# Optimization experiments

Hardware: AMD Instinct MI355X
Metric: run time of the kernel (lower is better)

Reference implementation:

```python
import jax, jax.numpy as jnp
import numpy as np

DIM = 1024
HEADS = 16
HEAD_DIM = DIM // HEADS
SCALE = HEAD_DIM ** -0.5
EPS = 1e-5


def layernorm(x, g, b):
    mu = jnp.mean(x, axis=-1, keepdims=True)
    var = jnp.mean((x - mu) ** 2, axis=-1, keepdims=True)
    return (x - mu) * jax.lax.rsqrt(var + EPS) * g + b


def setup_inputs() -> dict:
    key = jax.random.key(0)
    ks = jax.random.split(key, 12)
    B, N = 2, 2048
    s = DIM ** -0.5
    return {
        "q": jax.random.normal(ks[0], (B, N, DIM), jnp.float32),
        "k": jax.random.normal(ks[1], (B, N, DIM), jnp.float32),
        "v": jax.random.normal(ks[2], (B, N, DIM), jnp.float32),
        "gq": jnp.ones((DIM,), jnp.float32), "bq_ln": jnp.zeros((DIM,), jnp.float32),
        "gk": jnp.ones((DIM,), jnp.float32), "bk_ln": jnp.zeros((DIM,), jnp.float32),
        "gv": jnp.ones((DIM,), jnp.float32), "bv_ln": jnp.zeros((DIM,), jnp.float32),
        "Wq": jax.random.normal(ks[3], (DIM, DIM), jnp.float32) * s,
        "bq": jnp.zeros((DIM,), jnp.float32),
        "Wk": jax.random.normal(ks[4], (DIM, DIM), jnp.float32) * s,
        "bk": jnp.zeros((DIM,), jnp.float32),
        "Wv": jax.random.normal(ks[5], (DIM, DIM), jnp.float32) * s,
        "bv": jnp.zeros((DIM,), jnp.float32),
        "Wp": jax.random.normal(ks[6], (DIM, DIM), jnp.float32) * s,
        "bp": jnp.zeros((DIM,), jnp.float32),
    }


def reference(q, k, v, gq, bq_ln, gk, bk_ln, gv, bv_ln, Wq, bq, Wk, bk, Wv, bv, Wp, bp):
    B, Nq, C = q.shape
    Nk, Nv = k.shape[1], v.shape[1]
    qn = layernorm(q, gq, bq_ln)
    kn = layernorm(k, gk, bk_ln)
    vn = layernorm(v, gv, bv_ln)
    # project and split heads -> [B, H, N, hd]
    qh = (qn @ Wq + bq).reshape(B, Nq, HEADS, HEAD_DIM).transpose(0, 2, 1, 3)
    kh = (kn @ Wk + bk).reshape(B, Nk, HEADS, HEAD_DIM).transpose(0, 2, 1, 3)
    vh = (vn @ Wv + bv).reshape(B, Nv, HEADS, HEAD_DIM).transpose(0, 2, 1, 3)
    attn = jnp.einsum("bhqd,bhkd->bhqk", qh, kh) * SCALE
    attn = jax.nn.softmax(attn, axis=-1)
    out = jnp.einsum("bhqk,bhkd->bhqd", attn, vh)
    out = out.transpose(0, 2, 1, 3).reshape(B, Nq, C)
    out = out @ Wp + bp
    return (out, kh, vh)
```

## Files before the change

kernel.cpp:

```cpp
#include <hip/hip_runtime.h>
#include <cstdint>

#define DIMC 1024
#define NSEQ 2048
#define BATCH 2
#define HEADS 16
#define HD 64
#define MROWS (BATCH * NSEQ)

typedef unsigned short u16;
typedef unsigned int u32;
typedef __attribute__((ext_vector_type(8))) short bf16x8;
typedef __attribute__((ext_vector_type(4))) float f32x4;

#if __has_builtin(__builtin_amdgcn_exp2f)
#define EXP2(x) __builtin_amdgcn_exp2f(x)
#else
#define EXP2(x) exp2f(x)
#endif

__device__ __forceinline__ u16 f2bf(float f) {
  union { float f; u32 u; } v; v.f = f;
  u32 u = v.u;
  return (u16)((u + 0x7fffu + ((u >> 16) & 1u)) >> 16);
}
__device__ __forceinline__ u32 pack_rne(float a, float b) {
  return (u32)f2bf(a) | ((u32)f2bf(b) << 16);
}
__device__ __forceinline__ u32 pack_trunc(float a, float b) {
  union { float f; u32 u; } x, y; x.f = a; y.f = b;
  return (x.u >> 16) | (y.u & 0xffff0000u);
}
__device__ __forceinline__ void gload_lds16(const void* g, void* l) {
  __builtin_amdgcn_global_load_lds((const __attribute__((address_space(1))) void*)g,
                                   (__attribute__((address_space(3))) void*)l, 16, 0, 0);
}

__global__ __launch_bounds__(256)
void prep(const float* __restrict__ q, const float* __restrict__ k,
          const float* __restrict__ v,
          const float* __restrict__ gq, const float* __restrict__ bq,
          const float* __restrict__ gk, const float* __restrict__ bk,
          const float* __restrict__ gv, const float* __restrict__ bv,
          const float* __restrict__ w0, const float* __restrict__ w1,
          const float* __restrict__ w2, const float* __restrict__ w3,
          u16* __restrict__ xn, u16* __restrict__ wtout) {
  __shared__ float rs[4], rs2[4];
  __shared__ float tile[32][33];
  int tid = threadIdx.x;
  if (blockIdx.x < 3 * MROWS) {
    int rowid = blockIdx.x;
    int tensor = rowid >> 12;
    int r = rowid & 4095;
    const float *src, *g, *b;
    if (tensor == 0)      { src = q; g = gq; b = bq; }
    else if (tensor == 1) { src = k; g = gk; b = bk; }
    else                  { src = v; g = gv; b = bv; }
    src += (size_t)r * DIMC;
    u16* dst = xn + (size_t)tensor * MROWS * DIMC + (size_t)r * DIMC;
    float4 x = ((const float4*)src)[tid];
    float s  = x.x + x.y + x.z + x.w;
    float s2 = x.x*x.x + x.y*x.y + x.z*x.z + x.w*x.w;
    #pragma unroll
    for (int m = 1; m < 64; m <<= 1) { s += __shfl_xor(s, m); s2 += __shfl_xor(s2, m); }
    int wave = tid >> 6, lane = tid & 63;
    if (lane == 0) { rs[wave] = s; rs2[wave] = s2; }
    __syncthreads();
    s  = rs[0] + rs[1] + rs[2] + rs[3];
    s2 = rs2[0] + rs2[1] + rs2[2] + rs2[3];
    float mu  = s * (1.0f / DIMC);
    float var = s2 * (1.0f / DIMC) - mu * mu;
    float inv = rsqrtf(var + 1e-5f);
    float4 gg = ((const float4*)g)[tid];
    float4 bb = ((const float4*)b)[tid];
    uint2 o;
    o.x = pack_rne((x.x - mu) * inv * gg.x + bb.x, (x.y - mu) * inv * gg.y + bb.y);
    o.y = pack_rne((x.z - mu) * inv * gg.z + bb.z, (x.w - mu) * inv * gg.w + bb.w);
    ((uint2*)dst)[tid] = o;
  } else {
    int blk = blockIdx.x - 3 * MROWS;
    int widx = blk >> 10, t = blk & 1023;
    int ti = t >> 5, tj = t & 31;
    const float* W = (widx == 0) ? w0 : (widx == 1) ? w1 : (widx == 2) ? w2 : w3;
    u16* O = wtout + (size_t)widx * DIMC * DIMC;
    int tx = tid & 31, ty = tid >> 5;
    #pragma unroll
    for (int rr = 0; rr < 32; rr += 8)
      tile[ty + rr][tx] = W[(size_t)(ti * 32 + ty + rr) * DIMC + tj * 32 + tx];
    __syncthreads();
    #pragma unroll
    for (int rr = 0; rr < 32; rr += 8)
      O[(size_t)(tj * 32 + ty + rr) * DIMC + ti * 32 + tx] = f2bf(tile[tx][ty + rr]);
  }
}

__global__ __launch_bounds__(256)
void qkv_gemm(const u16* __restrict__ xn, const u16* __restrict__ wt,
              const float* __restrict__ bq, const float* __restrict__ bk,
              const float* __restrict__ bv,
              float* __restrict__ out, u16* __restrict__ qh,
              u16* __restrict__ khb, u16* __restrict__ vtb) {
  __shared__ u16 smem[128 * 136];
  u16* As = smem;
  u16* Bs = smem + 4096;
  u16* Ls = smem;
  const int z = blockIdx.z;
  const u16* A  = xn + (size_t)z * MROWS * DIMC;
  const u16* Bt = wt + (size_t)z * DIMC * DIMC;
  const float* bias = (z == 0) ? bq : (z == 1) ? bk : bv;
  const int bm = blockIdx.x, bn = blockIdx.y;
  const int tid = threadIdx.x;
  const int wave = tid >> 6, lane = tid & 63;
  const int wm = (wave & 1) * 64, wn = (wave >> 1) * 64;
  const int row = lane & 15, quad = lane >> 4;
  const float QSCL = 0.18033688011112042f;
  f32x4 acc[4][4] = {};
  for (int k0 = 0; k0 < DIMC; k0 += 32) {
    #pragma unroll
    for (int c = 0; c < 2; ++c) {
      int e = c * 2048 + tid * 8;
      int rr = e >> 5, col = e & 31;
      gload_lds16(&A[(size_t)(bm * 128 + rr) * DIMC + k0 + col], &As[e]);
      gload_lds16(&Bt[(size_t)(bn * 128 + rr) * DIMC + k0 + col], &Bs[e]);
    }
    __syncthreads();
    bf16x8 a[4], b[4];
    #pragma unroll
    for (int i = 0; i < 4; ++i)
      a[i] = *(const bf16x8*)(&As[(wm + i * 16 + row) * 32 + quad * 8]);
    #pragma unroll
    for (int j = 0; j < 4; ++j)
      b[j] = *(const bf16x8*)(&Bs[(wn + j * 16 + row) * 32 + quad * 8]);
    #pragma unroll
    for (int i = 0; i < 4; ++i)
      #pragma unroll
      for (int j = 0; j < 4; ++j)
        acc[i][j] = __builtin_amdgcn_mfma_f32_16x16x32_bf16(a[i], b[j], acc[i][j], 0, 0, 0);
    __syncthreads();
  }
  #pragma unroll
  for (int i = 0; i < 4; ++i) {
    #pragma unroll
    for (int j = 0; j < 4; ++j) {
      float val[4];
      #pragma unroll
      for (int r = 0; r < 4; ++r) {
        int m = bm * 128 + wm + i * 16 + quad * 4 + r;
        int c = bn * 128 + wn + j * 16 + row;
        val[r] = acc[i][j][r] + bias[c];
        int b_ = m >> 11, n = m & 2047, h = c >> 6, d = c & 63;
        int bh = b_ * HEADS + h;
        size_t hidx = ((size_t)bh * NSEQ + n) * HD + d;
        if (z == 0) {
          qh[hidx] = f2bf(val[r] * QSCL);
        } else {
          out[(size_t)z * MROWS * DIMC + hidx] = val[r];
          if (z == 1) khb[hidx] = f2bf(val[r]);
        }
      }
      if (z == 2) {
        int ct = wn + j * 16 + row;
        int mt = wm + i * 16 + quad * 4;
        u32* L = (u32*)(&Ls[ct * 136 + mt]);
        L[0] = pack_rne(val[0], val[1]);
        L[1] = pack_rne(val[2], val[3]);
      }
    }
  }
  if (z == 2) {
    __syncthreads();
    int b_ = (bm * 128) >> 11;
    int nbase = (bm * 128) & 2047;
    #pragma unroll
    for (int it = 0; it < 8; ++it) {
      int idx = it * 256 + tid;
      int ct = idx >> 4, ch = idx & 15;
      uint4 y = *(const uint4*)(&Ls[ct * 136 + ch * 8]);
      int c = bn * 128 + ct;
      int h = c >> 6, d = c & 63;
      size_t o = ((size_t)(b_ * HEADS + h) * HD + d) * NSEQ + nbase + ch * 8;
      *(uint4*)(&vtb[o]) = y;
    }
  }
}

__global__ __launch_bounds__(256)
void out_gemm(const u16* __restrict__ A, const u16* __restrict__ Bt,
              const float* __restrict__ bias, float* __restrict__ outf) {
  __shared__ u16 As[64 * 32];
  __shared__ u16 Bs[128 * 32];
  const int bm = blockIdx.x, bn = blockIdx.y;
  const int tid = threadIdx.x;
  const int wave = tid >> 6, lane = tid & 63;
  const int wm = (wave & 1) * 32, wn = (wave >> 1) * 64;
  const int row = lane & 15, quad = lane >> 4;
  f32x4 acc[2][4] = {};
  for (int k0 = 0; k0 < DIMC; k0 += 32) {
    {
      int e = tid * 8;
      int rr = e >> 5, col = e & 31;
      gload_lds16(&A[(size_t)(bm * 64 + rr) * DIMC + k0 + col], &As[e]);
    }
    #pragma unroll
    for (int c = 0; c < 2; ++c) {
      int e = c * 2048 + tid * 8;
      int rr = e >> 5, col = e & 31;
      gload_lds16(&Bt[(size_t)(bn * 128 + rr) * DIMC + k0 + col], &Bs[e]);
    }
    __syncthreads();
    bf16x8 a[2], b[4];
    #pragma unroll
    for (int i = 0; i < 2; ++i)
      a[i] = *(const bf16x8*)(&As[(wm + i * 16 + row) * 32 + quad * 8]);
    #pragma unroll
    for (int j = 0; j < 4; ++j)
      b[j] = *(const bf16x8*)(&Bs[(wn + j * 16 + row) * 32 + quad * 8]);
    #pragma unroll
    for (int i = 0; i < 2; ++i)
      #pragma unroll
      for (int j = 0; j < 4; ++j)
        acc[i][j] = __builtin_amdgcn_mfma_f32_16x16x32_bf16(a[i], b[j], acc[i][j], 0, 0, 0);
    __syncthreads();
  }
  #pragma unroll
  for (int i = 0; i < 2; ++i)
    #pragma unroll
    for (int j = 0; j < 4; ++j)
      #pragma unroll
      for (int r = 0; r < 4; ++r) {
        int m = bm * 64 + wm + i * 16 + quad * 4 + r;
        int c = bn * 128 + wn + j * 16 + row;
        outf[(size_t)m * DIMC + c] = acc[i][j][r] + bias[c];
      }
}

__global__ __launch_bounds__(256)
void attn_fused(const u16* __restrict__ qh, const u16* __restrict__ kh,
                const u16* __restrict__ vt, u16* __restrict__ ao) {
  __shared__ u16 Ks[2][64 * 64];
  __shared__ u16 Vs[2][64 * 64];
  __shared__ u16 Ps[4][16 * 40];
  const int flat = blockIdx.x;
  const int bh = (flat & 7) * 4 + ((flat >> 3) & 3);
  const int qtile = flat >> 5;
  const int b = bh >> 4, h = bh & 15;
  const int tid = threadIdx.x;
  const int wave = tid >> 6, lane = tid & 63;
  const int qi = lane & 15, quad = lane >> 4;
  const int sw = qi & 7;
  const size_t base = (size_t)bh * NSEQ * HD;
  bf16x8 qf[2];
  {
    int qrow = qtile * 64 + wave * 16 + qi;
    #pragma unroll
    for (int kc = 0; kc < 2; ++kc)
      qf[kc] = *(const bf16x8*)(&qh[base + (size_t)qrow * HD + kc * 32 + quad * 8]);
  }
  #pragma unroll
  for (int c = 0; c < 2; ++c) {
    int p = c * 256 + tid;
    int rk = p >> 3, ck = p & 7;
    gload_lds16(&kh[base + (size_t)rk * HD + (ck ^ (rk & 7)) * 8], &Ks[0][p * 8]);
    gload_lds16(&vt[base + (size_t)rk * NSEQ + (ck ^ (rk & 7)) * 8], &Vs[0][p * 8]);
  }
  __syncthreads();
  float li = 0.f;
  f32x4 oacc[4] = {};
  u16* myPs = &Ps[wave][0];
  for (int t = 0; t < NSEQ / 64; ++t) {
    const int cur = t & 1;
    if (t < NSEQ / 64 - 1) {
      #pragma unroll
      for (int c = 0; c < 2; ++c) {
        int p = c * 256 + tid;
        int rk = p >> 3, ck = p & 7;
        gload_lds16(&kh[base + (size_t)((t + 1) * 64 + rk) * HD + (ck ^ (rk & 7)) * 8],
                    &Ks[cur ^ 1][p * 8]);
        gload_lds16(&vt[base + (size_t)rk * NSEQ + (t + 1) * 64 + (ck ^ (rk & 7)) * 8],
                    &Vs[cur ^ 1][p * 8]);
      }
    }
    const u16* Kb = &Ks[cur][0];
    const u16* Vb = &Vs[cur][0];
    #pragma unroll
    for (int kc = 0; kc < 2; ++kc) {
      f32x4 s0 = {}, s1 = {};
      {
        const u16* kr0 = &Kb[((kc * 2) * 16 + qi) * 64];
        const u16* kr1 = &Kb[((kc * 2 + 1) * 16 + qi) * 64];
        __builtin_amdgcn_s_setprio(1);
        s0 = __builtin_amdgcn_mfma_f32_16x16x32_bf16(
            *(const bf16x8*)(&kr0[(quad ^ sw) * 8]), qf[0], s0, 0, 0, 0);
        s0 = __builtin_amdgcn_mfma_f32_16x16x32_bf16(
            *(const bf16x8*)(&kr0[((4 + quad) ^ sw) * 8]), qf[1], s0, 0, 0, 0);
        s1 = __builtin_amdgcn_mfma_f32_16x16x32_bf16(
            *(const bf16x8*)(&kr1[(quad ^ sw) * 8]), qf[0], s1, 0, 0, 0);
        s1 = __builtin_amdgcn_mfma_f32_16x16x32_bf16(
            *(const bf16x8*)(&kr1[((4 + quad) ^ sw) * 8]), qf[1], s1, 0, 0, 0);
        __builtin_amdgcn_s_setprio(0);
      }
      float p0 = EXP2(s0[0]), p1 = EXP2(s0[1]), p2 = EXP2(s0[2]), p3 = EXP2(s0[3]);
      float p4 = EXP2(s1[0]), p5 = EXP2(s1[1]), p6 = EXP2(s1[2]), p7 = EXP2(s1[3]);
      float psum = ((p0 + p1) + (p2 + p3)) + ((p4 + p5) + (p6 + p7));
      {
        u32* w0 = (u32*)(&myPs[qi * 40 + quad * 4]);
        w0[0] = pack_trunc(p0, p1);
        w0[1] = pack_trunc(p2, p3);
        u32* w1 = (u32*)(&myPs[qi * 40 + 16 + quad * 4]);
        w1[0] = pack_trunc(p4, p5);
        w1[1] = pack_trunc(p6, p7);
      }
      psum += __shfl_xor(psum, 16);
      psum += __shfl_xor(psum, 32);
      li += psum;
      asm volatile("" ::: "memory");
      bf16x8 pf = *(const bf16x8*)(&myPs[qi * 40 + quad * 8]);
      __builtin_amdgcn_s_setprio(1);
      #pragma unroll
      for (int dt = 0; dt < 4; ++dt) {
        bf16x8 vf = *(const bf16x8*)(&Vb[(dt * 16 + qi) * 64 + ((kc * 4 + quad) ^ sw) * 8]);
        oacc[dt] = __builtin_amdgcn_mfma_f32_16x16x32_bf16(vf, pf, oacc[dt], 0, 0, 0);
      }
      __builtin_amdgcn_s_setprio(0);
    }
    __syncthreads();
  }
  {
    float inv = 1.0f / li;
    int token = b * NSEQ + qtile * 64 + wave * 16 + qi;
    #pragma unroll
    for (int dt = 0; dt < 4; ++dt) {
      int col = h * 64 + dt * 16 + quad * 4;
      *(u32*)(&ao[(size_t)token * DIMC + col])     = pack_rne(oacc[dt][0] * inv, oacc[dt][1] * inv);
      *(u32*)(&ao[(size_t)token * DIMC + col + 2]) = pack_rne(oacc[dt][2] * inv, oacc[dt][3] * inv);
    }
  }
}

extern "C" void kernel_launch(void* const* d_in, const int* in_sizes, int n_in,
                              void* d_out, int out_size, void* d_ws, size_t ws_size,
                              hipStream_t stream) {
  const float* q    = (const float*)d_in[0];
  const float* k    = (const float*)d_in[1];
  const float* v    = (const float*)d_in[2];
  const float* gq   = (const float*)d_in[3];
  const float* bqln = (const float*)d_in[4];
  const float* gk   = (const float*)d_in[5];
  const float* bkln = (const float*)d_in[6];
  const float* gv   = (const float*)d_in[7];
  const float* bvln = (const float*)d_in[8];
  const float* Wq   = (const float*)d_in[9];
  const float* bq   = (const float*)d_in[10];
  const float* Wk   = (const float*)d_in[11];
  const float* bk   = (const float*)d_in[12];
  const float* Wv   = (const float*)d_in[13];
  const float* bv   = (const float*)d_in[14];
  const float* Wp   = (const float*)d_in[15];
  const float* bp   = (const float*)d_in[16];
  float* out = (float*)d_out;

  char* ws = (char*)d_ws;
  u16* xn  = (u16*)(ws);
  u16* wt  = (u16*)(ws + (size_t)25165824);
  u16* qh  = (u16*)(ws + (size_t)33554432);
  u16* khb = (u16*)(ws + (size_t)41943040);
  u16* ao  = (u16*)(ws + (size_t)50331648);
  u16* vtb = (u16*)d_out;

  const size_t WEL = (size_t)DIMC * DIMC;

  prep<<<3 * MROWS + 4096, 256, 0, stream>>>(q, k, v, gq, bqln, gk, bkln, gv, bvln,
                                             Wq, Wk, Wv, Wp, xn, wt);
  qkv_gemm<<<dim3(MROWS / 128, DIMC / 128, 3), 256, 0, stream>>>(
      xn, wt, bq, bk, bv, out, qh, khb, vtb);
  attn_fused<<<dim3((NSEQ / 64) * BATCH * HEADS), 256, 0, stream>>>(qh, khb, vtb, ao);
  out_gemm<<<dim3(MROWS / 64, DIMC / 128), 256, 0, stream>>>(ao, wt + 3 * WEL, bp, out);
}
```

Before: 256.3 us.

## Process two query sub-tiles per wave to reuse K/V tiles in attention

```diff
diff --git a/kernel.cpp b/kernel.cpp
--- a/kernel.cpp
+++ b/kernel.cpp
@@ -239,7 +239,7 @@
                 const u16* __restrict__ vt, u16* __restrict__ ao) {
   __shared__ u16 Ks[2][64 * 64];
   __shared__ u16 Vs[2][64 * 64];
-  __shared__ u16 Ps[4][16 * 40];
+  __shared__ u16 Ps[4][2][16 * 40];
   const int flat = blockIdx.x;
   const int bh = (flat & 7) * 4 + ((flat >> 3) & 3);
   const int qtile = flat >> 5;
@@ -249,12 +249,13 @@
   const int qi = lane & 15, quad = lane >> 4;
   const int sw = qi & 7;
   const size_t base = (size_t)bh * NSEQ * HD;
-  bf16x8 qf[2];
-  {
-    int qrow = qtile * 64 + wave * 16 + qi;
-    #pragma unroll
-    for (int kc = 0; kc < 2; ++kc)
-      qf[kc] = *(const bf16x8*)(&qh[base + (size_t)qrow * HD + kc * 32 + quad * 8]);
+  bf16x8 qf[2][2];
+  #pragma unroll
+  for (int qt = 0; qt < 2; ++qt) {
+    int qrow = qtile * 128 + wave * 32 + qt * 16 + qi;
+    #pragma unroll
+    for (int kc2 = 0; kc2 < 2; ++kc2)
+      qf[qt][kc2] = *(const bf16x8*)(&qh[base + (size_t)qrow * HD + kc2 * 32 + quad * 8]);
   }
   #pragma unroll
   for (int c = 0; c < 2; ++c) {
@@ -264,9 +265,10 @@
     gload_lds16(&vt[base + (size_t)rk * NSEQ + (ck ^ (rk & 7)) * 8], &Vs[0][p * 8]);
   }
   __syncthreads();
-  float li = 0.f;
-  f32x4 oacc[4] = {};
-  u16* myPs = &Ps[wave][0];
+  float li0 = 0.f, li1 = 0.f;
+  f32x4 oacc[2][4] = {};
+  u16* P0 = &Ps[wave][0][0];
+  u16* P1 = &Ps[wave][1][0];
   for (int t = 0; t < NSEQ / 64; ++t) {
     const int cur = t & 1;
     if (t < NSEQ / 64 - 1) {
@@ -284,55 +286,67 @@
     const u16* Vb = &Vs[cur][0];
     #pragma unroll
     for (int kc = 0; kc < 2; ++kc) {
-      f32x4 s0 = {}, s1 = {};
+      const u16* kr0 = &Kb[((kc * 2) * 16 + qi) * 64];
+      const u16* kr1 = &Kb[((kc * 2 + 1) * 16 + qi) * 64];
+      bf16x8 ka0 = *(const bf16x8*)(&kr0[(quad ^ sw) * 8]);
+      bf16x8 ka1 = *(const bf16x8*)(&kr0[((4 + quad) ^ sw) * 8]);
+      bf16x8 kb0 = *(const bf16x8*)(&kr1[(quad ^ sw) * 8]);
+      bf16x8 kb1 = *(const bf16x8*)(&kr1[((4 + quad) ^ sw) * 8]);
+      f32x4 s00 = {}, s01 = {}, s10 = {}, s11 = {};
+      __builtin_amdgcn_s_setprio(1);
+      s00 = __builtin_amdgcn_mfma_f32_16x16x32_bf16(ka0, qf[0][0], s00, 0, 0, 0);
+      s00 = __builtin_amdgcn_mfma_f32_16x16x32_bf16(ka1, qf[0][1], s00, 0, 0, 0);
+      s01 = __builtin_amdgcn_mfma_f32_16x16x32_bf16(kb0, qf[0][0], s01, 0, 0, 0);
+      s01 = __builtin_amdgcn_mfma_f32_16x16x32_bf16(kb1, qf[0][1], s01, 0, 0, 0);
+      s10 = __builtin_amdgcn_mfma_f32_16x16x32_bf16(ka0, qf[1][0], s10, 0, 0, 0);
+      s10 = __builtin_amdgcn_mfma_f32_16x16x32_bf16(ka1, qf[1][1], s10, 0, 0, 0);
+      s11 = __builtin_amdgcn_mfma_f32_16x16x32_bf16(kb0, qf[1][0], s11, 0, 0, 0);
+      s11 = __builtin_amdgcn_mfma_f32_16x16x32_bf16(kb1, qf[1][1], s11, 0, 0, 0);
+      __builtin_amdgcn_s_setprio(0);
+      float a0 = EXP2(s00[0]), a1 = EXP2(s00[1]), a2 = EXP2(s00[2]), a3 = EXP2(s00[3]);
+      float a4 = EXP2(s01[0]), a5 = EXP2(s01[1]), a6 = EXP2(s01[2]), a7 = EXP2(s01[3]);
+      float b0 = EXP2(s10[0]), b1 = EXP2(s10[1]), b2 = EXP2(s10[2]), b3 = EXP2(s10[3]);
+      float b4 = EXP2(s11[0]), b5 = EXP2(s11[1]), b6 = EXP2(s11[2]), b7 = EXP2(s11[3]);
+      li0 += ((a0 + a1) + (a2 + a3)) + ((a4 + a5) + (a6 + a7));
+      li1 += ((b0 + b1) + (b2 + b3)) + ((b4 + b5) + (b6 + b7));
       {
-        const u16* kr0 = &Kb[((kc * 2) * 16 + qi) * 64];
-        const u16* kr1 = &Kb[((kc * 2 + 1) * 16 + qi) * 64];
-        __builtin_amdgcn_s_setprio(1);
-        s0 = __builtin_amdgcn_mfma_f32_16x16x32_bf16(
-            *(const bf16x8*)(&kr0[(quad ^ sw) * 8]), qf[0], s0, 0, 0, 0);
-        s0 = __builtin_amdgcn_mfma_f32_16x16x32_bf16(
-            *(const bf16x8*)(&kr0[((4 + quad) ^ sw) * 8]), qf[1], s0, 0, 0, 0);
-        s1 = __builtin_amdgcn_mfma_f32_16x16x32_bf16(
-            *(const bf16x8*)(&kr1[(quad ^ sw) * 8]), qf[0], s1, 0, 0, 0);
-        s1 = __builtin_amdgcn_mfma_f32_16x16x32_bf16(
-            *(const bf16x8*)(&kr1[((4 + quad) ^ sw) * 8]), qf[1], s1, 0, 0, 0);
-        __builtin_amdgcn_s_setprio(0);
-      }
-      float p0 = EXP2(s0[0]), p1 = EXP2(s0[1]), p2 = EXP2(s0[2]), p3 = EXP2(s0[3]);
-      float p4 = EXP2(s1[0]), p5 = EXP2(s1[1]), p6 = EXP2(s1[2]), p7 = EXP2(s1[3]);
-      float psum = ((p0 + p1) + (p2 + p3)) + ((p4 + p5) + (p6 + p7));
-      {
-        u32* w0 = (u32*)(&myPs[qi * 40 + quad * 4]);
-        w0[0] = pack_trunc(p0, p1);
-        w0[1] = pack_trunc(p2, p3);
-        u32* w1 = (u32*)(&myPs[qi * 40 + 16 + quad * 4]);
-        w1[0] = pack_trunc(p4, p5);
-        w1[1] = pack_trunc(p6, p7);
-      }
-      psum += __shfl_xor(psum, 16);
-      psum += __shfl_xor(psum, 32);
-      li += psum;
+        uint2 w;
+        w.x = pack_trunc(a0, a1); w.y = pack_trunc(a2, a3);
+        *(uint2*)(&P0[qi * 40 + quad * 4]) = w;
+        w.x = pack_trunc(a4, a5); w.y = pack_trunc(a6, a7);
+        *(uint2*)(&P0[qi * 40 + 16 + quad * 4]) = w;
+        w.x = pack_trunc(b0, b1); w.y = pack_trunc(b2, b3);
+        *(uint2*)(&P1[qi * 40 + quad * 4]) = w;
+        w.x = pack_trunc(b4, b5); w.y = pack_trunc(b6, b7);
+        *(uint2*)(&P1[qi * 40 + 16 + quad * 4]) = w;
+      }
       asm volatile("" ::: "memory");
-      bf16x8 pf = *(const bf16x8*)(&myPs[qi * 40 + quad * 8]);
+      bf16x8 pf0 = *(const bf16x8*)(&P0[qi * 40 + quad * 8]);
+      bf16x8 pf1 = *(const bf16x8*)(&P1[qi * 40 + quad * 8]);
       __builtin_amdgcn_s_setprio(1);
       #pragma unroll
       for (int dt = 0; dt < 4; ++dt) {
         bf16x8 vf = *(const bf16x8*)(&Vb[(dt * 16 + qi) * 64 + ((kc * 4 + quad) ^ sw) * 8]);
-        oacc[dt] = __builtin_amdgcn_mfma_f32_16x16x32_bf16(vf, pf, oacc[dt], 0, 0, 0);
+        oacc[0][dt] = __builtin_amdgcn_mfma_f32_16x16x32_bf16(vf, pf0, oacc[0][dt], 0, 0, 0);
+        oacc[1][dt] = __builtin_amdgcn_mfma_f32_16x16x32_bf16(vf, pf1, oacc[1][dt], 0, 0, 0);
       }
       __builtin_amdgcn_s_setprio(0);
     }
     __syncthreads();
   }
-  {
-    float inv = 1.0f / li;
-    int token = b * NSEQ + qtile * 64 + wave * 16 + qi;
+  li0 += __shfl_xor(li0, 16); li0 += __shfl_xor(li0, 32);
+  li1 += __shfl_xor(li1, 16); li1 += __shfl_xor(li1, 32);
+  #pragma unroll
+  for (int qt = 0; qt < 2; ++qt) {
+    float inv = 1.0f / (qt == 0 ? li0 : li1);
+    int token = b * NSEQ + qtile * 128 + wave * 32 + qt * 16 + qi;
     #pragma unroll
     for (int dt = 0; dt < 4; ++dt) {
       int col = h * 64 + dt * 16 + quad * 4;
-      *(u32*)(&ao[(size_t)token * DIMC + col])     = pack_rne(oacc[dt][0] * inv, oacc[dt][1] * inv);
-      *(u32*)(&ao[(size_t)token * DIMC + col + 2]) = pack_rne(oacc[dt][2] * inv, oacc[dt][3] * inv);
+      *(u32*)(&ao[(size_t)token * DIMC + col]) =
+          pack_rne(oacc[qt][dt][0] * inv, oacc[qt][dt][1] * inv);
+      *(u32*)(&ao[(size_t)token * DIMC + col + 2]) =
+          pack_rne(oacc[qt][dt][2] * inv, oacc[qt][dt][3] * inv);
     }
   }
 }
@@ -373,6 +387,6 @@
                                              Wq, Wk, Wv, Wp, xn, wt);
   qkv_gemm<<<dim3(MROWS / 128, DIMC / 128, 3), 256, 0, stream>>>(
       xn, wt, bq, bk, bv, out, qh, khb, vtb);
-  attn_fused<<<dim3((NSEQ / 64) * BATCH * HEADS), 256, 0, stream>>>(qh, khb, vtb, ao);
+  attn_fused<<<dim3((NSEQ / 128) * BATCH * HEADS), 256, 0, stream>>>(qh, khb, vtb, ao);
   out_gemm<<<dim3(MROWS / 64, DIMC / 128), 256, 0, stream>>>(ao, wt + 3 * WEL, bp, out);
 }
```

Measured after the change: 244.2 us. 1.05x faster.
